# Optimization experiments

Measured on AMD Instinct MI355X. Metric: run time of the kernel, lower is better.

The kernel has to match this reference:

```python
import jax, jax.numpy as jnp
import numpy as np

B, I, O, N = 65536, 256, 32, 8


def chebyshev_basis(x, n):
    """Chebyshev polynomials T_0..T_{n-1} of x. x: [B, I] -> [B, I, n]."""
    T = [jnp.ones_like(x), x]
    for _ in range(n - 2):
        T.append(2.0 * x * T[-1] - T[-2])
    return jnp.stack(T[:n], axis=-1)


def setup_inputs() -> dict:
    key = jax.random.key(0)
    k1, k2 = jax.random.split(key)
    # inputs live on [-1, 1], the natural Chebyshev domain
    x = jax.random.uniform(k1, (B, I), jnp.float32, minval=-1.0, maxval=1.0)
    # weight init mirrors torch: uniform(-weight_magnitude/in, weight_magnitude/in)
    w = jax.random.uniform(k2, (O, I, N), jnp.float32, minval=-1.0 / I, maxval=1.0 / I)
    return {"x": x, "w": w}


def reference(x, w):
    n = w.shape[-1]
    phi = chebyshev_basis(x, n)          # [B, I, n] basis expansion
    out = jnp.einsum("bin,oin->bo", phi, w)  # weighted contraction
    return out
```

## Files before the change

### kernel.cpp

```cpp
#include <hip/hip_runtime.h>
#include <hip/hip_bf16.h>


typedef __attribute__((ext_vector_type(8)))  short bf16x8;
typedef __attribute__((ext_vector_type(16))) float f32x16;
typedef __attribute__((ext_vector_type(4)))  float f32x4;

__device__ __forceinline__ short f2b(float f) {
    __hip_bfloat16 h = __float2bfloat16(f);
    short s;
    __builtin_memcpy(&s, &h, sizeof(s));
    return s;
}

__device__ __forceinline__ unsigned pkbf_tr(float lo, float hi) {
    unsigned a, b;
    __builtin_memcpy(&a, &hi, 4);
    __builtin_memcpy(&b, &lo, 4);
    return __builtin_amdgcn_perm(a, b, 0x07060302u);
}

__global__ __launch_bounds__(256) void prep_w_kernel(const float* __restrict__ w,
                                                     short* __restrict__ wB) {
    int idx = blockIdx.x * 256 + threadIdx.x;
    int kc2 = idx >> 9;
    int l   = (idx >> 3) & 63;
    int jj  = idx & 7;
    int o = l & 31, g = l >> 5;
    int i = 2 * kc2 + (jj >> 2);
    int n = 4 * g + (jj & 3);
    wB[idx] = f2b(w[(o * 256 + i) * 8 + n]);
}

__global__ __launch_bounds__(256, 5) void cheb_mm_kernel(const float* __restrict__ x,
                                                         const short* __restrict__ wB,
                                                         float* __restrict__ out) {
    __shared__ float smem[8192];
    const int tid = threadIdx.x;
    const int wv  = tid >> 6;
    const int l   = tid & 63;
    const int g   = l >> 5;
    const int r0  = l & 31;
    const long long rowB = (long long)blockIdx.x * 32;

    const bf16x8* wq = (const bf16x8*)wB + wv * 2048 + l;
    bf16x8 bfc[4];
    #pragma unroll
    for (int p = 0; p < 4; ++p) bfc[p] = wq[p * 64];

    {
        const float4* xg4 = (const float4*)(x + rowB * 256);
        const int f4l = l & 15;
        const int rsub = l >> 4;
        float4 stg[8];
        #pragma unroll
        for (int q = 0; q < 8; ++q)
            stg[q] = xg4[(q * 4 + rsub) * 64 + wv * 16 + f4l];
        #pragma unroll
        for (int q = 0; q < 8; ++q) {
            const int row  = q * 4 + rsub;
            const int base = row * 256 + wv * 64;
            const int s    = row & 31;
            const int p0 = 2 * f4l, p1 = 2 * f4l + 1;
            *(float2*)&smem[base + 2 * (p0 ^ s)] = make_float2(stg[q].x, stg[q].y);
            *(float2*)&smem[base + 2 * (p1 ^ s)] = make_float2(stg[q].z, stg[q].w);
        }
    }

    f32x16 accA{}, accB{};
    const float* sf = smem;
    const int base0 = r0 * 256 + wv * 64 + g + (r0 << 1);

    float xc[4];
    #pragma unroll
    for (int i0 = 0; i0 < 4; ++i0) xc[i0] = sf[base0 ^ (i0 << 1)];

    #pragma unroll
    for (int t = 0; t < 32; ++t) {
        const bf16x8 bfrag = bfc[t & 3];
        const float  xv    = xc[t & 3];
        if (t + 4 < 32) {
            bfc[t & 3] = wq[(t + 4) * 64];
            xc[t & 3]  = sf[base0 ^ ((t + 4) << 1)];
        }

        const float x2 = xv + xv;
        const float T2 = fmaf(x2, xv, -1.f);
        const float T3 = fmaf(x2, T2, -xv);
        const float T4 = fmaf(x2, T3, -T2);
        const float T5 = fmaf(x2, T4, -T3);
        const float T6 = fmaf(x2, T5, -T4);
        const float T7 = fmaf(x2, T6, -T5);
        unsigned R0 = pkbf_tr(1.f, xv);
        unsigned R1 = pkbf_tr(T2, T3);
        unsigned R2 = pkbf_tr(T4, T5);
        unsigned R3 = pkbf_tr(T6, T7);
        auto r02 = __builtin_amdgcn_permlane32_swap(R0, R2, false, false);
        auto r13 = __builtin_amdgcn_permlane32_swap(R1, R3, false, false);
        union { unsigned u[4]; bf16x8 v; } af;
        af.u[0] = r02[0]; af.u[1] = r13[0];
        af.u[2] = r02[1]; af.u[3] = r13[1];
        if (t & 1)
            accB = __builtin_amdgcn_mfma_f32_32x32x16_bf16(af.v, bfrag, accB, 0, 0, 0);
        else
            accA = __builtin_amdgcn_mfma_f32_32x32x16_bf16(af.v, bfrag, accA, 0, 0, 0);
    }
    const f32x16 acc = accA + accB;

    #pragma unroll
    for (int r = 0; r < 16; ++r) {
        const int rloc = (r & 3) + 8 * (r >> 2) + 4 * g;
        smem[rloc * 256 + wv * 64 + r0] = acc[r];
    }
    __syncthreads();

    {
        float* op = out + rowB * 32;
        const int f   = tid * 4;
        const int row = f >> 5;
        const int c   = f & 31;
        const int b   = row * 256 + c;
        f32x4 v0 = *(const f32x4*)&smem[b];
        f32x4 v1 = *(const f32x4*)&smem[b + 64];
        f32x4 v2 = *(const f32x4*)&smem[b + 128];
        f32x4 v3 = *(const f32x4*)&smem[b + 192];
        f32x4 s = (v0 + v1) + (v2 + v3);
        *(f32x4*)(op + f) = s;
    }
}

extern "C" void kernel_launch(void* const* d_in, const int* in_sizes, int n_in,
                              void* d_out, int out_size, void* d_ws, size_t ws_size,
                              hipStream_t stream) {
    const float* x = (const float*)d_in[0];
    const float* w = (const float*)d_in[1];
    float* out = (float*)d_out;
    short* wB = (short*)d_ws;

    prep_w_kernel<<<256, 256, 0, stream>>>(w, wB);
    cheb_mm_kernel<<<2048, 256, 0, stream>>>(x, wB, out);
}
```

Baseline: 29.10 us.

## Load x directly from global into registers, bypassing shared memory staging

Replaces the cooperative staging of x into swizzled shared memory with per-lane float4 global loads that are prefetched four steps ahead inside the MFMA loop. This removes the LDS write/read round trip for the input and halves shared memory to 4096 floats, which is now used only for the cross-wave output reduction with a simpler layout. The trade-off is that each lane's global loads now stride across rows (row-per-lane), which coalesces less well than the previous row-contiguous loads and relies on caches to absorb the access pattern.

```diff
diff --git a/kernel.cpp b/kernel.cpp
--- a/kernel.cpp
+++ b/kernel.cpp
@@ -35,7 +35,7 @@
 __global__ __launch_bounds__(256, 5) void cheb_mm_kernel(const float* __restrict__ x,
                                                          const short* __restrict__ wB,
                                                          float* __restrict__ out) {
-    __shared__ float smem[8192];
+    __shared__ float smem[4096];
     const int tid = threadIdx.x;
     const int wv  = tid >> 6;
     const int l   = tid & 63;
@@ -43,46 +43,26 @@
     const int r0  = l & 31;
     const long long rowB = (long long)blockIdx.x * 32;
 
-    const bf16x8* wq = (const bf16x8*)wB + wv * 2048 + l;
+    const float4* xrow = (const float4*)x + (rowB + r0) * 64 + wv * 16;
+    const bf16x8* wq   = (const bf16x8*)wB + wv * 2048 + l;
+
     bf16x8 bfc[4];
     #pragma unroll
     for (int p = 0; p < 4; ++p) bfc[p] = wq[p * 64];
-
-    {
-        const float4* xg4 = (const float4*)(x + rowB * 256);
-        const int f4l = l & 15;
-        const int rsub = l >> 4;
-        float4 stg[8];
-        #pragma unroll
-        for (int q = 0; q < 8; ++q)
-            stg[q] = xg4[(q * 4 + rsub) * 64 + wv * 16 + f4l];
-        #pragma unroll
-        for (int q = 0; q < 8; ++q) {
-            const int row  = q * 4 + rsub;
-            const int base = row * 256 + wv * 64;
-            const int s    = row & 31;
-            const int p0 = 2 * f4l, p1 = 2 * f4l + 1;
-            *(float2*)&smem[base + 2 * (p0 ^ s)] = make_float2(stg[q].x, stg[q].y);
-            *(float2*)&smem[base + 2 * (p1 ^ s)] = make_float2(stg[q].z, stg[q].w);
-        }
-    }
+    float4 xq[4];
+    #pragma unroll
+    for (int p = 0; p < 4; ++p) xq[p] = xrow[p];
 
     f32x16 accA{}, accB{};
-    const float* sf = smem;
-    const int base0 = r0 * 256 + wv * 64 + g + (r0 << 1);
-
-    float xc[4];
-    #pragma unroll
-    for (int i0 = 0; i0 < 4; ++i0) xc[i0] = sf[base0 ^ (i0 << 1)];
 
     #pragma unroll
     for (int t = 0; t < 32; ++t) {
+        const int cc = t >> 1;
+        const float4 f4 = xq[cc & 3];
+        const float xv = (t & 1) ? (g ? f4.w : f4.z) : (g ? f4.y : f4.x);
         const bf16x8 bfrag = bfc[t & 3];
-        const float  xv    = xc[t & 3];
-        if (t + 4 < 32) {
-            bfc[t & 3] = wq[(t + 4) * 64];
-            xc[t & 3]  = sf[base0 ^ ((t + 4) << 1)];
-        }
+        if (t + 4 < 32) bfc[t & 3] = wq[(t + 4) * 64];
+        if ((t & 1) && cc + 4 < 16) xq[cc & 3] = xrow[cc + 4];
 
         const float x2 = xv + xv;
         const float T2 = fmaf(x2, xv, -1.f);
@@ -110,20 +90,17 @@
     #pragma unroll
     for (int r = 0; r < 16; ++r) {
         const int rloc = (r & 3) + 8 * (r >> 2) + 4 * g;
-        smem[rloc * 256 + wv * 64 + r0] = acc[r];
+        smem[wv * 1024 + rloc * 32 + r0] = acc[r];
     }
     __syncthreads();
 
     {
         float* op = out + rowB * 32;
-        const int f   = tid * 4;
-        const int row = f >> 5;
-        const int c   = f & 31;
-        const int b   = row * 256 + c;
-        f32x4 v0 = *(const f32x4*)&smem[b];
-        f32x4 v1 = *(const f32x4*)&smem[b + 64];
-        f32x4 v2 = *(const f32x4*)&smem[b + 128];
-        f32x4 v3 = *(const f32x4*)&smem[b + 192];
+        const int f = tid * 4;
+        f32x4 v0 = *(const f32x4*)&smem[f];
+        f32x4 v1 = *(const f32x4*)&smem[1024 + f];
+        f32x4 v2 = *(const f32x4*)&smem[2048 + f];
+        f32x4 v3 = *(const f32x4*)&smem[3072 + f];
         f32x4 s = (v0 + v1) + (v2 + v3);
         *(f32x4*)(op + f) = s;
     }
```

Measured after the change: 41.69 us. 1.43x slower.

## Pipeline x staging into LDS in chunks overlapped with MFMA compute

Applied to the files above, without the earlier changes.

The up-front load of the block's whole x tile into shared memory (eight float4 per thread) is replaced by four column chunks. Each chunk is loaded from global memory while the previous chunk's Chebyshev expansion and MFMAs run, then written into the wave's own swizzled LDS slice. The aim is to hide global load latency behind compute and to cut the staging register footprint from eight float4 to two. In exchange the control flow gets more complex, and correctness depends on each wave reading only LDS rows it wrote itself, since there is no barrier between the writes and the reads.

```diff
diff --git a/kernel.cpp b/kernel.cpp
--- a/kernel.cpp
+++ b/kernel.cpp
@@ -44,66 +44,82 @@
     const long long rowB = (long long)blockIdx.x * 32;
 
     const bf16x8* wq = (const bf16x8*)wB + wv * 2048 + l;
+    const float4* xg4 = (const float4*)(x + rowB * 256);
+    const float* sf = smem;
+
+    const int rA = l >> 2;
+    const int sA = l & 3;
+    float4 st0, st1;
+
+    auto ISSUE = [&](int c) {
+        const int f4c = wv * 16 + 4 * c + sA;
+        st0 = xg4[rA * 64 + f4c];
+        st1 = xg4[(rA + 16) * 64 + f4c];
+    };
+    auto WRITE = [&](int c) {
+        const int f4l = 4 * c + sA;
+        const int p0 = 2 * f4l, p1 = p0 + 1;
+        {
+            const int base = rA * 256 + wv * 64, s = rA & 31;
+            *(float2*)&smem[base + 2 * (p0 ^ s)] = make_float2(st0.x, st0.y);
+            *(float2*)&smem[base + 2 * (p1 ^ s)] = make_float2(st0.z, st0.w);
+        }
+        {
+            const int base = (rA + 16) * 256 + wv * 64, s = (rA + 16) & 31;
+            *(float2*)&smem[base + 2 * (p0 ^ s)] = make_float2(st1.x, st1.y);
+            *(float2*)&smem[base + 2 * (p1 ^ s)] = make_float2(st1.z, st1.w);
+        }
+    };
+
+    ISSUE(0);
     bf16x8 bfc[4];
     #pragma unroll
     for (int p = 0; p < 4; ++p) bfc[p] = wq[p * 64];
 
-    {
-        const float4* xg4 = (const float4*)(x + rowB * 256);
-        const int f4l = l & 15;
-        const int rsub = l >> 4;
-        float4 stg[8];
-        #pragma unroll
-        for (int q = 0; q < 8; ++q)
-            stg[q] = xg4[(q * 4 + rsub) * 64 + wv * 16 + f4l];
-        #pragma unroll
-        for (int q = 0; q < 8; ++q) {
-            const int row  = q * 4 + rsub;
-            const int base = row * 256 + wv * 64;
-            const int s    = row & 31;
-            const int p0 = 2 * f4l, p1 = 2 * f4l + 1;
-            *(float2*)&smem[base + 2 * (p0 ^ s)] = make_float2(stg[q].x, stg[q].y);
-            *(float2*)&smem[base + 2 * (p1 ^ s)] = make_float2(stg[q].z, stg[q].w);
-        }
-    }
-
     f32x16 accA{}, accB{};
-    const float* sf = smem;
     const int base0 = r0 * 256 + wv * 64 + g + (r0 << 1);
 
-    float xc[4];
-    #pragma unroll
-    for (int i0 = 0; i0 < 4; ++i0) xc[i0] = sf[base0 ^ (i0 << 1)];
+    WRITE(0);
+    ISSUE(1);
 
     #pragma unroll
-    for (int t = 0; t < 32; ++t) {
-        const bf16x8 bfrag = bfc[t & 3];
-        const float  xv    = xc[t & 3];
-        if (t + 4 < 32) {
-            bfc[t & 3] = wq[(t + 4) * 64];
-            xc[t & 3]  = sf[base0 ^ ((t + 4) << 1)];
+    for (int c = 0; c < 4; ++c) {
+        float xc[4];
+        #pragma unroll
+        for (int j = 0; j < 4; ++j) xc[j] = sf[base0 ^ ((8 * c + j) << 1)];
+        #pragma unroll
+        for (int j = 0; j < 8; ++j) {
+            const int t = 8 * c + j;
+            const bf16x8 bfrag = bfc[t & 3];
+            const float  xv    = xc[j & 3];
+            if (t + 4 < 32) bfc[t & 3] = wq[(t + 4) * 64];
+            if (j + 4 < 8)  xc[j & 3]  = sf[base0 ^ ((t + 4) << 1)];
+
+            const float x2 = xv + xv;
+            const float T2 = fmaf(x2, xv, -1.f);
+            const float T3 = fmaf(x2, T2, -xv);
+            const float T4 = fmaf(x2, T3, -T2);
+            const float T5 = fmaf(x2, T4, -T3);
+            const float T6 = fmaf(x2, T5, -T4);
+            const float T7 = fmaf(x2, T6, -T5);
+            unsigned R0 = pkbf_tr(1.f, xv);
+            unsigned R1 = pkbf_tr(T2, T3);
+            unsigned R2 = pkbf_tr(T4, T5);
+            unsigned R3 = pkbf_tr(T6, T7);
+            auto r02 = __builtin_amdgcn_permlane32_swap(R0, R2, false, false);
+            auto r13 = __builtin_amdgcn_permlane32_swap(R1, R3, false, false);
+            union { unsigned u[4]; bf16x8 v; } af;
+            af.u[0] = r02[0]; af.u[1] = r13[0];
+            af.u[2] = r02[1]; af.u[3] = r13[1];
+            if (t & 1)
+                accB = __builtin_amdgcn_mfma_f32_32x32x16_bf16(af.v, bfrag, accB, 0, 0, 0);
+            else
+                accA = __builtin_amdgcn_mfma_f32_32x32x16_bf16(af.v, bfrag, accA, 0, 0, 0);
         }
-
-        const float x2 = xv + xv;
-        const float T2 = fmaf(x2, xv, -1.f);
-        const float T3 = fmaf(x2, T2, -xv);
-        const float T4 = fmaf(x2, T3, -T2);
-        const float T5 = fmaf(x2, T4, -T3);
-        const float T6 = fmaf(x2, T5, -T4);
-        const float T7 = fmaf(x2, T6, -T5);
-        unsigned R0 = pkbf_tr(1.f, xv);
-        unsigned R1 = pkbf_tr(T2, T3);
-        unsigned R2 = pkbf_tr(T4, T5);
-        unsigned R3 = pkbf_tr(T6, T7);
-        auto r02 = __builtin_amdgcn_permlane32_swap(R0, R2, false, false);
-        auto r13 = __builtin_amdgcn_permlane32_swap(R1, R3, false, false);
-        union { unsigned u[4]; bf16x8 v; } af;
-        af.u[0] = r02[0]; af.u[1] = r13[0];
-        af.u[2] = r02[1]; af.u[3] = r13[1];
-        if (t & 1)
-            accB = __builtin_amdgcn_mfma_f32_32x32x16_bf16(af.v, bfrag, accB, 0, 0, 0);
-        else
-            accA = __builtin_amdgcn_mfma_f32_32x32x16_bf16(af.v, bfrag, accA, 0, 0, 0);
+        if (c < 3) {
+            WRITE(c + 1);
+            if (c < 2) ISSUE(c + 2);
+        }
     }
     const f32x16 acc = accA + accB;
 
@@ -118,8 +134,8 @@
         float* op = out + rowB * 32;
         const int f   = tid * 4;
         const int row = f >> 5;
-        const int c   = f & 31;
-        const int b   = row * 256 + c;
+        const int c2  = f & 31;
+        const int b   = row * 256 + c2;
         f32x4 v0 = *(const f32x4*)&smem[b];
         f32x4 v1 = *(const f32x4*)&smem[b + 64];
         f32x4 v2 = *(const f32x4*)&smem[b + 128];
```

Result: no change. 29.37 us (+0.9%).

## Process two row tiles per block, prefetching second x tile and preloading all weights

Applied to the files above, without the earlier changes.

Each block now handles two 32-row tiles: it preloads all 32 weight fragments into registers once and issues global loads for the second tile's x while computing the first. This hides x-load latency behind MFMA work and halves weight reloads per row. In exchange it raises register pressure (128 VGPRs of weights plus staging), lowers the occupancy hint from 5 to 4, and halves the grid to 1024 blocks.

```diff
diff --git a/kernel.cpp b/kernel.cpp
--- a/kernel.cpp
+++ b/kernel.cpp
@@ -32,7 +32,7 @@
     wB[idx] = f2b(w[(o * 256 + i) * 8 + n]);
 }
 
-__global__ __launch_bounds__(256, 5) void cheb_mm_kernel(const float* __restrict__ x,
+__global__ __launch_bounds__(256, 4) void cheb_mm_kernel(const float* __restrict__ x,
                                                          const short* __restrict__ wB,
                                                          float* __restrict__ out) {
     __shared__ float smem[8192];
@@ -41,21 +41,18 @@
     const int l   = tid & 63;
     const int g   = l >> 5;
     const int r0  = l & 31;
-    const long long rowB = (long long)blockIdx.x * 32;
+    const int f4l = l & 15;
+    const int rsub = l >> 4;
 
-    const bf16x8* wq = (const bf16x8*)wB + wv * 2048 + l;
-    bf16x8 bfc[4];
-    #pragma unroll
-    for (int p = 0; p < 4; ++p) bfc[p] = wq[p * 64];
+    float4 stg[8];
 
-    {
+    auto ISSUE = [&](long long rowB) {
         const float4* xg4 = (const float4*)(x + rowB * 256);
-        const int f4l = l & 15;
-        const int rsub = l >> 4;
-        float4 stg[8];
         #pragma unroll
         for (int q = 0; q < 8; ++q)
             stg[q] = xg4[(q * 4 + rsub) * 64 + wv * 16 + f4l];
+    };
+    auto WRITE = [&]() {
         #pragma unroll
         for (int q = 0; q < 8; ++q) {
             const int row  = q * 4 + rsub;
@@ -65,67 +62,87 @@
             *(float2*)&smem[base + 2 * (p0 ^ s)] = make_float2(stg[q].x, stg[q].y);
             *(float2*)&smem[base + 2 * (p1 ^ s)] = make_float2(stg[q].z, stg[q].w);
         }
-    }
+    };
 
-    f32x16 accA{}, accB{};
+    const long long rowB0 = (long long)blockIdx.x * 32;
+    const long long rowB1 = (long long)(blockIdx.x + 1024) * 32;
+
+    ISSUE(rowB0);
+
+    const bf16x8* wq = (const bf16x8*)wB + wv * 2048 + l;
+    bf16x8 ball[32];
+    #pragma unroll
+    for (int t = 0; t < 32; ++t) ball[t] = wq[t * 64];
+
+    WRITE();
+    ISSUE(rowB1);
+
     const float* sf = smem;
     const int base0 = r0 * 256 + wv * 64 + g + (r0 << 1);
 
-    float xc[4];
     #pragma unroll
-    for (int i0 = 0; i0 < 4; ++i0) xc[i0] = sf[base0 ^ (i0 << 1)];
+    for (int tile = 0; tile < 2; ++tile) {
+        const long long rowB = tile ? rowB1 : rowB0;
 
-    #pragma unroll
-    for (int t = 0; t < 32; ++t) {
-        const bf16x8 bfrag = bfc[t & 3];
-        const float  xv    = xc[t & 3];
-        if (t + 4 < 32) {
-            bfc[t & 3] = wq[(t + 4) * 64];
-            xc[t & 3]  = sf[base0 ^ ((t + 4) << 1)];
+        f32x16 accA{}, accB{};
+        float xc[4];
+        #pragma unroll
+        for (int j = 0; j < 4; ++j) xc[j] = sf[base0 ^ (j << 1)];
+
+        #pragma unroll
+        for (int t = 0; t < 32; ++t) {
+            const bf16x8 bfrag = ball[t];
+            const float  xv    = xc[t & 3];
+            if (t + 4 < 32) xc[t & 3] = sf[base0 ^ ((t + 4) << 1)];
+
+            const float x2 = xv + xv;
+            const float T2 = fmaf(x2, xv, -1.f);
+            const float T3 = fmaf(x2, T2, -xv);
+            const float T4 = fmaf(x2, T3, -T2);
+            const float T5 = fmaf(x2, T4, -T3);
+            const float T6 = fmaf(x2, T5, -T4);
+            const float T7 = fmaf(x2, T6, -T5);
+            unsigned R0 = pkbf_tr(1.f, xv);
+            unsigned R1 = pkbf_tr(T2, T3);
+            unsigned R2 = pkbf_tr(T4, T5);
+            unsigned R3 = pkbf_tr(T6, T7);
+            auto r02 = __builtin_amdgcn_permlane32_swap(R0, R2, false, false);
+            auto r13 = __builtin_amdgcn_permlane32_swap(R1, R3, false, false);
+            union { unsigned u[4]; bf16x8 v; } af;
+            af.u[0] = r02[0]; af.u[1] = r13[0];
+            af.u[2] = r02[1]; af.u[3] = r13[1];
+            if (t & 1)
+                accB = __builtin_amdgcn_mfma_f32_32x32x16_bf16(af.v, bfrag, accB, 0, 0, 0);
+            else
+                accA = __builtin_amdgcn_mfma_f32_32x32x16_bf16(af.v, bfrag, accA, 0, 0, 0);
+        }
+        const f32x16 acc = accA + accB;
+
+        #pragma unroll
+        for (int r = 0; r < 16; ++r) {
+            const int rloc = (r & 3) + 8 * (r >> 2) + 4 * g;
+            smem[rloc * 256 + wv * 64 + r0] = acc[r];
+        }
+        __syncthreads();
+
+        {
+            float* op = out + rowB * 32;
+            const int f   = tid * 4;
+            const int row = f >> 5;
+            const int c2  = f & 31;
+            const int b   = row * 256 + c2;
+            f32x4 v0 = *(const f32x4*)&smem[b];
+            f32x4 v1 = *(const f32x4*)&smem[b + 64];
+            f32x4 v2 = *(const f32x4*)&smem[b + 128];
+            f32x4 v3 = *(const f32x4*)&smem[b + 192];
+            f32x4 s = (v0 + v1) + (v2 + v3);
+            *(f32x4*)(op + f) = s;
         }
 
-        const float x2 = xv + xv;
-        const float T2 = fmaf(x2, xv, -1.f);
-        const float T3 = fmaf(x2, T2, -xv);
-        const float T4 = fmaf(x2, T3, -T2);
-        const float T5 = fmaf(x2, T4, -T3);
-        const float T6 = fmaf(x2, T5, -T4);
-        const float T7 = fmaf(x2, T6, -T5);
-        unsigned R0 = pkbf_tr(1.f, xv);
-        unsigned R1 = pkbf_tr(T2, T3);
-        unsigned R2 = pkbf_tr(T4, T5);
-        unsigned R3 = pkbf_tr(T6, T7);
-        auto r02 = __builtin_amdgcn_permlane32_swap(R0, R2, false, false);
-        auto r13 = __builtin_amdgcn_permlane32_swap(R1, R3, false, false);
-        union { unsigned u[4]; bf16x8 v; } af;
-        af.u[0] = r02[0]; af.u[1] = r13[0];
-        af.u[2] = r02[1]; af.u[3] = r13[1];
-        if (t & 1)
-            accB = __builtin_amdgcn_mfma_f32_32x32x16_bf16(af.v, bfrag, accB, 0, 0, 0);
-        else
-            accA = __builtin_amdgcn_mfma_f32_32x32x16_bf16(af.v, bfrag, accA, 0, 0, 0);
-    }
-    const f32x16 acc = accA + accB;
-
-    #pragma unroll
-    for (int r = 0; r < 16; ++r) {
-        const int rloc = (r & 3) + 8 * (r >> 2) + 4 * g;
-        smem[rloc * 256 + wv * 64 + r0] = acc[r];
-    }
-    __syncthreads();
-
-    {
-        float* op = out + rowB * 32;
-        const int f   = tid * 4;
-        const int row = f >> 5;
-        const int c   = f & 31;
-        const int b   = row * 256 + c;
-        f32x4 v0 = *(const f32x4*)&smem[b];
-        f32x4 v1 = *(const f32x4*)&smem[b + 64];
-        f32x4 v2 = *(const f32x4*)&smem[b + 128];
-        f32x4 v3 = *(const f32x4*)&smem[b + 192];
-        f32x4 s = (v0 + v1) + (v2 + v3);
-        *(f32x4*)(op + f) = s;
+        if (tile == 0) {
+            __syncthreads();
+            WRITE();
+        }
     }
 }
 
@@ -138,5 +155,5 @@
     short* wB = (short*)d_ws;
 
     prep_w_kernel<<<256, 256, 0, stream>>>(w, wB);
-    cheb_mm_kernel<<<2048, 256, 0, stream>>>(x, wB, out);
+    cheb_mm_kernel<<<1024, 256, 0, stream>>>(x, wB, out);
 }
```

Result: slower. 69.78 us (+139.8%).
